# Performance work log

Measured on AMD Instinct MI355X. Metric: run time of the kernel, lower is better.

The kernel has to match this reference:

```python
import jax, jax.numpy as jnp
import numpy as np

P = 2048  # number of problems


def _structure():
    # Symbols per problem alternate 128/384; questions per problem alternate 32/96.
    p = np.arange(P)
    S = np.where(p % 2 == 0, 128, 384).astype(np.int64)   # num_symbols per problem
    Q = np.where(p % 2 == 0, 32, 96).astype(np.int64)     # num_questions per problem
    cost_starts = np.concatenate([[0], np.cumsum(S)])[:-1]  # row starts into costs_flat
    prob_of_question = np.repeat(p, Q)                     # [T_Q] problem id of each question
    S_per_q = np.repeat(S, Q)                              # [T_Q] symbols per question
    TQ = S_per_q.shape[0]
    qs_segment = np.repeat(np.arange(TQ), S_per_q)         # [T_total] question id of each element
    q_elem_starts = np.concatenate([[0], np.cumsum(S_per_q)])[:-1]
    T = qs_segment.shape[0]
    # offset of each element within its question, then add that problem's cost row start
    offsets = np.arange(T) - np.repeat(q_elem_starts, S_per_q)
    starts_per_q = np.repeat(cost_starts, Q)
    cost_index = np.repeat(starts_per_q, S_per_q) + offsets  # tile_like gather indices
    return (cost_index.astype(np.int32), qs_segment.astype(np.int32),
            prob_of_question.astype(np.int32))


def setup_inputs() -> dict:
    key = jax.random.key(0)
    k1, k2, k3 = jax.random.split(key, 3)
    cost_index, qs_segment, prob_of_question = _structure()
    T = cost_index.shape[0]            # 41_943_040
    TS = (P // 2) * (128 + 384)        # 524_288
    occ_flat = jax.random.uniform(k1, (T,), dtype=jnp.float32)   # occurrence counts >= 0
    costs_flat = jax.random.normal(k2, (TS,), dtype=jnp.float32)  # symbol costs (weights)
    valid = jax.random.uniform(k3, (P,)) < 0.9                    # per-problem valid mask
    return {
        'occ_flat': occ_flat,
        'costs_flat': costs_flat,
        'valid': valid,
        'cost_index': jnp.asarray(cost_index),
        'qs_segment': jnp.asarray(qs_segment),
        'prob_of_question': jnp.asarray(prob_of_question),
    }


def reference(occ_flat, costs_flat, valid, cost_index, qs_segment, prob_of_question):
    # tile_like: broadcast each problem's costs to each of its questions (gather)
    # costs_to_logits: elementwise multiply + per-question reduce_sum
    # costs_decorated_to_logits: invalid problems' logits are 0 (scatter_nd into zeros)
    TQ = prob_of_question.shape[0]
    potentials = occ_flat * costs_flat[cost_index]             # [T_total]
    logits_q = jax.ops.segment_sum(potentials, qs_segment, num_segments=TQ)  # [T_Q]
    return jnp.where(valid[prob_of_question], logits_q, jnp.zeros((), logits_q.dtype))
```

## Files before the change

kernel.cpp:

```cpp
#include <hip/hip_runtime.h>


typedef float f4 __attribute__((ext_vector_type(4)));

__device__ __forceinline__ float dot4(f4 a, f4 b) {
    return a.x * b.x + a.y * b.y + a.z * b.z + a.w * b.w;
}

__global__ __launch_bounds__(256)
void classifier_kernel(const float* __restrict__ occ,
                       const float* __restrict__ costs,
                       const void*  __restrict__ valid,
                       float* __restrict__ out) {
    const int lane  = threadIdx.x & 31;
    const int flane = threadIdx.x & 63;

    unsigned int w = ((const unsigned int*)valid)[flane];
    const bool u8 = (__ballot(w > 1u) != 0ull);

    const int g    = blockIdx.x;
    const int pair = ((g >> 6) << 3) | (g & 7);
    const int sub  = (g >> 3) & 7;
    const int k    = (sub << 3) | (int)(threadIdx.x >> 5);

    const float* pbase = occ + 40960 * pair;

    float s0 = 0.0f, s1 = 0.0f;
    int qa, qb;
    if (k < 16) {
        const int j = k;
        qa = 128 * pair + j;
        qb = qa + 16;
        const int prob = 2 * pair;
        const bool v = u8 ? (((const unsigned char*)valid)[prob] != 0)
                          : (((const int*)valid)[prob] != 0);
        if (v) {
            const f4* o0 = (const f4*)(pbase + 128 * j);
            const f4* o1 = (const f4*)(pbase + 128 * (j + 16));
            const f4* c  = (const f4*)(costs + 512 * pair);
            f4 a0 = __builtin_nontemporal_load(&o0[lane]);
            f4 a1 = __builtin_nontemporal_load(&o1[lane]);
            f4 b  = c[lane];
            s0 = dot4(a0, b);
            s1 = dot4(a1, b);
        }
    } else {
        const int j = k - 16;
        qa = 128 * pair + 32 + j;
        qb = qa + 48;
        const int prob = 2 * pair + 1;
        const bool v = u8 ? (((const unsigned char*)valid)[prob] != 0)
                          : (((const int*)valid)[prob] != 0);
        if (v) {
            const f4* o0 = (const f4*)(pbase + 4096 + 384 * j);
            const f4* o1 = (const f4*)(pbase + 4096 + 384 * (j + 48));
            const f4* c  = (const f4*)(costs + 512 * pair + 128);
            f4 a00 = __builtin_nontemporal_load(&o0[lane]);
            f4 a01 = __builtin_nontemporal_load(&o0[lane + 32]);
            f4 a02 = __builtin_nontemporal_load(&o0[lane + 64]);
            f4 a10 = __builtin_nontemporal_load(&o1[lane]);
            f4 a11 = __builtin_nontemporal_load(&o1[lane + 32]);
            f4 a12 = __builtin_nontemporal_load(&o1[lane + 64]);
            f4 b0  = c[lane];
            f4 b1  = c[lane + 32];
            f4 b2  = c[lane + 64];
            s0 = dot4(a00, b0) + dot4(a01, b1) + dot4(a02, b2);
            s1 = dot4(a10, b0) + dot4(a11, b1) + dot4(a12, b2);
        }
    }

    #pragma unroll
    for (int off = 16; off > 0; off >>= 1) {
        s0 += __shfl_down(s0, off, 32);
        s1 += __shfl_down(s1, off, 32);
    }

    if (lane == 0) {
        out[qa] = s0;
        out[qb] = s1;
    }
}

extern "C" void kernel_launch(void* const* d_in, const int* in_sizes, int n_in,
                              void* d_out, int out_size, void* d_ws, size_t ws_size,
                              hipStream_t stream) {
    const float* occ   = (const float*)d_in[0];
    const float* costs = (const float*)d_in[1];
    const void*  valid = (const void*)d_in[2];

    const int TQ      = out_size;
    const int threads = (TQ / 2) * 32;
    const int block   = 256;
    const int grid    = threads / block;

    classifier_kernel<<<grid, block, 0, stream>>>(occ, costs, valid, (float*)d_out);
}
```

Before: 344.5 us.

## Restructure work split so each half-wave handles multiple questions with LDS-staged costs

Reorganizes the grid into groups of 9 blocks: 8 blocks handle the 384-symbol problems, with each half-wave computing 3 questions, and 1 block handles the 128-symbol problems of two pairs, with each half-wave computing 8 questions. Cost vectors are staged once per block in shared memory rather than reloaded per half-wave. More loads are in flight per thread and the grid is smaller (4608 blocks). The trade-off is a __syncthreads per block, uneven work between the two block types, and a grid size hardcoded to the problem shape.

```diff
diff --git a/kernel.cpp b/kernel.cpp
--- a/kernel.cpp
+++ b/kernel.cpp
@@ -7,77 +7,96 @@
     return a.x * b.x + a.y * b.y + a.z * b.z + a.w * b.w;
 }
 
+__device__ __forceinline__ float hw_reduce(float s) {
+    #pragma unroll
+    for (int off = 16; off > 0; off >>= 1) s += __shfl_down(s, off, 32);
+    return s;
+}
+
 __global__ __launch_bounds__(256)
 void classifier_kernel(const float* __restrict__ occ,
                        const float* __restrict__ costs,
                        const void*  __restrict__ valid,
                        float* __restrict__ out) {
-    const int lane  = threadIdx.x & 31;
-    const int flane = threadIdx.x & 63;
+    __shared__ f4 lds_c[256];
+    const int tid   = threadIdx.x;
+    const int lane  = tid & 31;
+    const int hw    = tid >> 5;
+    const int flane = tid & 63;
 
-    unsigned int w = ((const unsigned int*)valid)[flane];
-    const bool u8 = (__ballot(w > 1u) != 0ull);
+    unsigned int wdet = ((const unsigned int*)valid)[flane];
+    const bool u8 = (__ballot(wdet > 1u) != 0ull);
 
-    const int g    = blockIdx.x;
-    const int pair = ((g >> 6) << 3) | (g & 7);
-    const int sub  = (g >> 3) & 7;
-    const int k    = (sub << 3) | (int)(threadIdx.x >> 5);
+    const int g     = blockIdx.x;
+    const int group = g / 9;
+    const int r     = g - group * 9;
 
-    const float* pbase = occ + 40960 * pair;
+    const f4* occ4  = (const f4*)occ;
+    const f4* cost4 = (const f4*)costs;
 
-    float s0 = 0.0f, s1 = 0.0f;
-    int qa, qb;
-    if (k < 16) {
-        const int j = k;
-        qa = 128 * pair + j;
-        qb = qa + 16;
-        const int prob = 2 * pair;
+    if (r < 8) {
+        const int pair  = 2 * group + (r & 1);
+        const int chunk = r >> 1;
+        const int prob  = 2 * pair + 1;
+        if (tid < 96) lds_c[tid] = cost4[128 * pair + 32 + tid];
+        __syncthreads();
         const bool v = u8 ? (((const unsigned char*)valid)[prob] != 0)
                           : (((const int*)valid)[prob] != 0);
+        const int j0 = 24 * chunk + 3 * hw;
+        float s0 = 0.0f, s1 = 0.0f, s2 = 0.0f;
         if (v) {
-            const f4* o0 = (const f4*)(pbase + 128 * j);
-            const f4* o1 = (const f4*)(pbase + 128 * (j + 16));
-            const f4* c  = (const f4*)(costs + 512 * pair);
-            f4 a0 = __builtin_nontemporal_load(&o0[lane]);
-            f4 a1 = __builtin_nontemporal_load(&o1[lane]);
-            f4 b  = c[lane];
-            s0 = dot4(a0, b);
-            s1 = dot4(a1, b);
+            f4 cb0 = lds_c[lane];
+            f4 cb1 = lds_c[lane + 32];
+            f4 cb2 = lds_c[lane + 64];
+            const f4* ob = occ4 + 10240 * pair + 1024 + 96 * j0 + lane;
+            f4 a0 = __builtin_nontemporal_load(ob);
+            f4 a1 = __builtin_nontemporal_load(ob + 32);
+            f4 a2 = __builtin_nontemporal_load(ob + 64);
+            f4 b0 = __builtin_nontemporal_load(ob + 96);
+            f4 b1 = __builtin_nontemporal_load(ob + 128);
+            f4 b2 = __builtin_nontemporal_load(ob + 160);
+            f4 c0 = __builtin_nontemporal_load(ob + 192);
+            f4 c1 = __builtin_nontemporal_load(ob + 224);
+            f4 c2 = __builtin_nontemporal_load(ob + 256);
+            s0 = dot4(a0, cb0) + dot4(a1, cb1) + dot4(a2, cb2);
+            s1 = dot4(b0, cb0) + dot4(b1, cb1) + dot4(b2, cb2);
+            s2 = dot4(c0, cb0) + dot4(c1, cb1) + dot4(c2, cb2);
+        }
+        s0 = hw_reduce(s0);
+        s1 = hw_reduce(s1);
+        s2 = hw_reduce(s2);
+        if (lane == 0) {
+            float* o = out + 128 * pair + 32 + j0;
+            o[0] = s0; o[1] = s1; o[2] = s2;
         }
     } else {
-        const int j = k - 16;
-        qa = 128 * pair + 32 + j;
-        qb = qa + 48;
-        const int prob = 2 * pair + 1;
+        const int e  = group;
+        const int pa = 2 * e, pb = 2 * e + 1;
+        lds_c[tid] = (tid < 128) ? cost4[128 * pa + tid]
+                                 : cost4[128 * pb + (tid - 128)];
+        __syncthreads();
+        const int p    = (hw < 4) ? pa : pb;
+        const int prob = 2 * p;
         const bool v = u8 ? (((const unsigned char*)valid)[prob] != 0)
                           : (((const int*)valid)[prob] != 0);
+        const int j0 = (hw & 3) * 8;
+        float s[8];
+        #pragma unroll
+        for (int i = 0; i < 8; ++i) s[i] = 0.0f;
         if (v) {
-            const f4* o0 = (const f4*)(pbase + 4096 + 384 * j);
-            const f4* o1 = (const f4*)(pbase + 4096 + 384 * (j + 48));
-            const f4* c  = (const f4*)(costs + 512 * pair + 128);
-            f4 a00 = __builtin_nontemporal_load(&o0[lane]);
-            f4 a01 = __builtin_nontemporal_load(&o0[lane + 32]);
-            f4 a02 = __builtin_nontemporal_load(&o0[lane + 64]);
-            f4 a10 = __builtin_nontemporal_load(&o1[lane]);
-            f4 a11 = __builtin_nontemporal_load(&o1[lane + 32]);
-            f4 a12 = __builtin_nontemporal_load(&o1[lane + 64]);
-            f4 b0  = c[lane];
-            f4 b1  = c[lane + 32];
-            f4 b2  = c[lane + 64];
-            s0 = dot4(a00, b0) + dot4(a01, b1) + dot4(a02, b2);
-            s1 = dot4(a10, b0) + dot4(a11, b1) + dot4(a12, b2);
+            f4 cb = lds_c[((hw < 4) ? 0 : 128) + lane];
+            const f4* ob = occ4 + 10240 * p + 32 * j0 + lane;
+            #pragma unroll
+            for (int i = 0; i < 8; ++i) {
+                f4 a = __builtin_nontemporal_load(ob + 32 * i);
+                s[i] = dot4(a, cb);
+            }
         }
-    }
-
-    #pragma unroll
-    for (int off = 16; off > 0; off >>= 1) {
-        s0 += __shfl_down(s0, off, 32);
-        s1 += __shfl_down(s1, off, 32);
-    }
-
-    if (lane == 0) {
-        out[qa] = s0;
-        out[qb] = s1;
+        #pragma unroll
+        for (int i = 0; i < 8; ++i) {
+            float sr = hw_reduce(s[i]);
+            if (lane == 0) out[128 * p + j0 + i] = sr;
+        }
     }
 }
 
@@ -88,10 +107,9 @@
     const float* costs = (const float*)d_in[1];
     const void*  valid = (const void*)d_in[2];
 
-    const int TQ      = out_size;
-    const int threads = (TQ / 2) * 32;
-    const int block   = 256;
-    const int grid    = threads / block;
+    (void)out_size;
+    const int grid  = 512 * 9;
+    const int block = 256;
 
     classifier_kernel<<<grid, block, 0, stream>>>(occ, costs, valid, (float*)d_out);
 }
```

Result: no change. 348.0 us (+1.0%).
